# Kernel optimization log

Hardware: AMD Instinct MI355X
Metric: run time of the kernel (lower is better)

Reference implementation:

```python
import jax, jax.numpy as jnp
import numpy as np

EPS = 1e-6  # model.epsilon


def setup_inputs() -> dict:
    key = jax.random.key(0)
    k1, k2 = jax.random.split(key)
    # X: one-hot-like translated sequence tensor [genomes, tiles, 6 frames, tile_len, alphabet]
    X = jax.random.uniform(k1, (8, 12, 6, 2000, 21), dtype=jnp.float32)
    Q = jnp.full((21,), 1.0 / 21.0, dtype=jnp.float32)  # background aa distribution
    # P_logit initialized like log(Q) + noise (matches _getRandomProfiles)
    P_logit = jnp.log(Q)[None, :, None] + 4.0 * jax.random.normal(k2, (8, 21, 48), dtype=jnp.float32)
    return {"X": X, "P_logit": P_logit, "Q": Q}


def reference(X, P_logit, Q):
    # P = softmax over alphabet axis; R = log odds vs background, clamped at epsilon
    P = jax.nn.softmax(P_logit, axis=1)                      # [k, A, U]
    R = jnp.log(jnp.maximum(P / Q[None, :, None], EPS))      # [k, A, U]
    D0, D1, D2, L, A = X.shape
    k, _, U = R.shape
    # conv2d with spatial (L, A), in_ch 1, out_ch U; width window covers full alphabet
    Xr = X.reshape(D0 * D1 * D2, L, A, 1)
    W = R.reshape(k, A, 1, U)
    Z = jax.lax.conv_general_dilated(
        Xr, W, window_strides=(1, 1), padding='VALID',
        dimension_numbers=('NHWC', 'HWIO', 'NHWC'))          # [B, L-k+1, 1, U]
    Z = Z.reshape(D0, D1, D2, L - k + 1, U)                  # [D0, D1, D2, P, U]
    S = jnp.max(Z, axis=(2, 3))                              # max over frames & positions -> [D0, D1, U]
    return (S, R, Z)
```

## Files before the change

### kernel.cpp

```cpp
#include <hip/hip_runtime.h>
#include <math.h>

typedef __attribute__((ext_vector_type(8))) short short8;
typedef __attribute__((ext_vector_type(4))) float f32x4;

#define D0n 8
#define D1n 12
#define D2n 6
#define Ln 2000
#define An 21
#define KPn 8
#define Un 48
#define PPn 1993
#define Bn 576
#define S_SIZE 4608
#define R_SIZE 8064

#define BPn 256
#define TILES 2
#define NBX 4
#define XROWS 264
#define XBUF_BYTES (XROWS * 64)
#define RB_BYTES (384 * 64)
#define BOFF (2 * XBUF_BYTES)
#define RED_OFF (BOFF + RB_BYTES)

__device__ __forceinline__ int swz(int b) { return b ^ ((b >> 2) & 0x70); }

__device__ __forceinline__ unsigned int fkey(float f) {
    unsigned int u = __float_as_uint(f);
    return (u & 0x80000000u) ? ~u : (u | 0x80000000u);
}
__device__ __forceinline__ float funkey(unsigned int k) {
    return __uint_as_float((k & 0x80000000u) ? (k ^ 0x80000000u) : ~k);
}
__device__ __forceinline__ unsigned short f2bf(float v) {
    unsigned int b = __float_as_uint(v);
    return (unsigned short)((b + 0x7FFFu + ((b >> 16) & 1u)) >> 16);
}

#define GLOAD_LDS16(g, l)                                                     \
    __builtin_amdgcn_global_load_lds(                                          \
        (const __attribute__((address_space(1))) void*)(g),                    \
        (__attribute__((address_space(3))) void*)(l), 16, 0, 0)

#define TILE_BARRIER()                                                        \
    do {                                                                      \
        asm volatile("s_waitcnt lgkmcnt(0)" ::: "memory");                    \
        __builtin_amdgcn_s_barrier();                                         \
        asm volatile("" ::: "memory");                                        \
    } while (0)

__global__ void k_profile(const float* __restrict__ P_logit,
                          const float* __restrict__ Q,
                          float* __restrict__ Rout,
                          unsigned short* __restrict__ Rb,
                          unsigned int* __restrict__ Skey) {
    int t = blockIdx.x * blockDim.x + threadIdx.x;
    if (t < S_SIZE) Skey[t] = 0u;
    if (t >= KPn * Un) return;
    int kp = t / Un, u = t % Un;
    const float* pl = P_logit + kp * (An * Un) + u;
    float v[An];
    float m = -INFINITY;
#pragma unroll
    for (int a = 0; a < An; ++a) { v[a] = pl[a * Un]; m = fmaxf(m, v[a]); }
    float s = 0.f;
#pragma unroll
    for (int a = 0; a < An; ++a) { v[a] = expf(v[a] - m); s += v[a]; }
    float inv = 1.f / s;
    int rowp = kp * Un + u;
#pragma unroll
    for (int a = 0; a < An; ++a) {
        float r = logf(fmaxf(v[a] * inv / Q[a], 1e-6f));
        Rout[(kp * An + a) * Un + u] = r;
        Rb[swz(rowp * 64 + a * 2) >> 1] = f2bf(r);
    }
#pragma unroll
    for (int a = An; a < 32; ++a) Rb[swz(rowp * 64 + a * 2) >> 1] = 0;
}

__device__ __forceinline__ void xwrite4(char* xbase, int idx, f32x4 g) {
    int fi = idx * 4;
    int row = fi / An;
    int a = fi - row * An;
#pragma unroll
    for (int e = 0; e < 4; ++e) {
        *(unsigned short*)(xbase + swz(row * 64 + a * 2)) = f2bf(g[e]);
        ++a;
        if (a == An) { a = 0; ++row; }
    }
}

__device__ __forceinline__ void xload(const float* __restrict__ X, int b,
                                      int tp0, int t, f32x4 g[3], int& n4) {
    int rows = min(XROWS, Ln - tp0);
    n4 = rows * An / 4;
    const f32x4* src = (const f32x4*)(X + ((size_t)b * Ln + tp0) * An);
#pragma unroll
    for (int i = 0; i < 3; ++i) {
        int idx = t + i * 512;
        g[i] = (idx < n4) ? src[idx] : (f32x4){0.f, 0.f, 0.f, 0.f};
    }
}

__device__ __forceinline__ void xstore(char* xbase, int t, const f32x4 g[3],
                                       int n4) {
#pragma unroll
    for (int i = 0; i < 3; ++i) {
        int idx = t + i * 512;
        if (idx < n4) xwrite4(xbase, idx, g[i]);
    }
}

__device__ __forceinline__ void qloop8(const char* smem, const char* xb,
                                       int lr, int ls, int pw,
                                       f32x4 acc[3][2]) {
#pragma unroll
    for (int q = 0; q < KPn; ++q) {
        const int rr = q * Un + lr;
        short8 rf0 = *(const short8*)(smem + BOFF + swz(rr * 64 + ls * 16));
        short8 rf1 = *(const short8*)(smem + BOFF + swz((rr + 16) * 64 + ls * 16));
        short8 rf2 = *(const short8*)(smem + BOFF + swz((rr + 32) * 64 + ls * 16));
        const int xr = pw + q + lr;
        short8 xf0 = *(const short8*)(xb + swz(xr * 64 + ls * 16));
        short8 xf1 = *(const short8*)(xb + swz((xr + 16) * 64 + ls * 16));
        acc[0][0] = __builtin_amdgcn_mfma_f32_16x16x32_bf16(rf0, xf0, acc[0][0], 0, 0, 0);
        acc[0][1] = __builtin_amdgcn_mfma_f32_16x16x32_bf16(rf0, xf1, acc[0][1], 0, 0, 0);
        acc[1][0] = __builtin_amdgcn_mfma_f32_16x16x32_bf16(rf1, xf0, acc[1][0], 0, 0, 0);
        acc[1][1] = __builtin_amdgcn_mfma_f32_16x16x32_bf16(rf1, xf1, acc[1][1], 0, 0, 0);
        acc[2][0] = __builtin_amdgcn_mfma_f32_16x16x32_bf16(rf2, xf0, acc[2][0], 0, 0, 0);
        acc[2][1] = __builtin_amdgcn_mfma_f32_16x16x32_bf16(rf2, xf1, acc[2][1], 0, 0, 0);
    }
}

__device__ __forceinline__ void store_tile(float* __restrict__ Z, int b,
                                           int tp0, int pw, int lr, int ls,
                                           const f32x4 acc[3][2],
                                           float smax[3][4]) {
#pragma unroll
    for (int np = 0; np < 2; ++np) {
        int p = tp0 + pw + np * 16 + lr;
        if (p < PPn) {
            float* zp = Z + ((size_t)b * PPn + p) * Un + ls * 4;
#pragma unroll
            for (int nu = 0; nu < 3; ++nu) {
                *(f32x4*)(zp + nu * 16) = acc[nu][np];
#pragma unroll
                for (int r = 0; r < 4; ++r)
                    smax[nu][r] = fmaxf(smax[nu][r], acc[nu][np][r]);
            }
        }
    }
}

__global__ __launch_bounds__(512, 4) void k_conv(
        const float* __restrict__ X,
        const unsigned short* __restrict__ Rb,
        float* __restrict__ Z,
        unsigned int* __restrict__ Skey) {
    __shared__ char smem[RED_OFF + 8 * Un * 4];
    const int b = blockIdx.y;
    const int base_p = blockIdx.x * (TILES * BPn);
    const int t = threadIdx.x;
    const int w = t >> 6;
    const int l = t & 63;
    const int lr = l & 15;
    const int ls = l >> 4;
    const int pw = w * 32;

    {
        const uint4* src = (const uint4*)Rb;
        uint4* dst = (uint4*)(smem + BOFF);
#pragma unroll
        for (int i = 0; i < RB_BYTES / 16 / 512; ++i) {
            int idx = t + i * 512;
            GLOAD_LDS16(src + idx, dst + idx);
        }
    }
    {
        uint4 z4 = {0u, 0u, 0u, 0u};
        uint4* xs = (uint4*)smem;
        for (int i = t; i < 2 * XBUF_BYTES / 16; i += 512) xs[i] = z4;
    }
    f32x4 g[3];
    int n4;
    xload(X, b, base_p, t, g, n4);
    __syncthreads();
    xstore((char*)smem, t, g, n4);
    TILE_BARRIER();

    float smax[3][4];
#pragma unroll
    for (int nu = 0; nu < 3; ++nu)
#pragma unroll
        for (int r = 0; r < 4; ++r) smax[nu][r] = -INFINITY;

    f32x4 acc[3][2];

    xload(X, b, base_p + BPn, t, g, n4);
#pragma unroll
    for (int nu = 0; nu < 3; ++nu)
#pragma unroll
        for (int np = 0; np < 2; ++np) acc[nu][np] = (f32x4){0.f, 0.f, 0.f, 0.f};
    qloop8((const char*)smem, (const char*)smem, lr, ls, pw, acc);
    xstore((char*)smem + XBUF_BYTES, t, g, n4);
    store_tile(Z, b, base_p, pw, lr, ls, acc, smax);
    TILE_BARRIER();

#pragma unroll
    for (int nu = 0; nu < 3; ++nu)
#pragma unroll
        for (int np = 0; np < 2; ++np) acc[nu][np] = (f32x4){0.f, 0.f, 0.f, 0.f};
    qloop8((const char*)smem, (const char*)smem + XBUF_BYTES, lr, ls, pw, acc);
    store_tile(Z, b, base_p + BPn, pw, lr, ls, acc, smax);

    float* red = (float*)(smem + RED_OFF);
#pragma unroll
    for (int nu = 0; nu < 3; ++nu)
#pragma unroll
        for (int r = 0; r < 4; ++r) {
            float v = smax[nu][r];
            v = fmaxf(v, __shfl_xor(v, 1));
            v = fmaxf(v, __shfl_xor(v, 2));
            v = fmaxf(v, __shfl_xor(v, 4));
            v = fmaxf(v, __shfl_xor(v, 8));
            if (lr == 0) red[w * Un + nu * 16 + ls * 4 + r] = v;
        }
    __syncthreads();
    if (t < Un) {
        float m = -INFINITY;
#pragma unroll
        for (int wv = 0; wv < 8; ++wv) m = fmaxf(m, red[wv * Un + t]);
        atomicMax(&Skey[(b / D2n) * Un + t], fkey(m));
    }
}

__global__ void k_decode(unsigned int* __restrict__ Skey) {
    int t = blockIdx.x * blockDim.x + threadIdx.x;
    if (t < S_SIZE) {
        float f = funkey(Skey[t]);
        ((float*)Skey)[t] = f;
    }
}

extern "C" void kernel_launch(void* const* d_in, const int* in_sizes, int n_in,
                              void* d_out, int out_size, void* d_ws, size_t ws_size,
                              hipStream_t stream) {
    const float* X = (const float*)d_in[0];
    const float* P_logit = (const float*)d_in[1];
    const float* Q = (const float*)d_in[2];

    float* S = (float*)d_out;
    float* Rout = S + S_SIZE;
    float* Z = Rout + R_SIZE;
    unsigned short* Rb = (unsigned short*)d_ws;

    k_profile<<<(S_SIZE + 63) / 64, 64, 0, stream>>>(P_logit, Q, Rout, Rb,
                                                     (unsigned int*)d_out);

    dim3 grid(NBX, Bn);
    k_conv<<<grid, 512, 0, stream>>>(X, Rb, Z, (unsigned int*)d_out);

    k_decode<<<(S_SIZE + 255) / 256, 256, 0, stream>>>((unsigned int*)d_out);
}
```

Before: 82.53 us.

## Use persistent blocks processing nine consecutive tiles with double-buffered X loads

Replaces the 4x576 grid of two-tile blocks with 512 persistent blocks, each walking 9 consecutive 256-position tiles across batch boundaries. The next tile's X is prefetched while the current one is computed, and the per-group max is flushed with an atomic only when the genome-tile group changes. This amortizes the per-block R staging into LDS and the launch/prologue cost, and balances the 4608 tiles over 512 blocks. In exchange, the flush adds extra barriers, and a block whose tiles span two groups pays for an additional reduction.

```diff
diff --git a/kernel.cpp b/kernel.cpp
--- a/kernel.cpp
+++ b/kernel.cpp
@@ -17,8 +17,8 @@
 #define R_SIZE 8064
 
 #define BPn 256
-#define TILES 2
-#define NBX 4
+#define NTIL 9
+#define NBLK 512
 #define XROWS 264
 #define XBUF_BYTES (XROWS * 64)
 #define RB_BYTES (384 * 64)
@@ -154,67 +154,10 @@
     }
 }
 
-__global__ __launch_bounds__(512, 4) void k_conv(
-        const float* __restrict__ X,
-        const unsigned short* __restrict__ Rb,
-        float* __restrict__ Z,
-        unsigned int* __restrict__ Skey) {
-    __shared__ char smem[RED_OFF + 8 * Un * 4];
-    const int b = blockIdx.y;
-    const int base_p = blockIdx.x * (TILES * BPn);
-    const int t = threadIdx.x;
-    const int w = t >> 6;
-    const int l = t & 63;
-    const int lr = l & 15;
-    const int ls = l >> 4;
-    const int pw = w * 32;
-
-    {
-        const uint4* src = (const uint4*)Rb;
-        uint4* dst = (uint4*)(smem + BOFF);
-#pragma unroll
-        for (int i = 0; i < RB_BYTES / 16 / 512; ++i) {
-            int idx = t + i * 512;
-            GLOAD_LDS16(src + idx, dst + idx);
-        }
-    }
-    {
-        uint4 z4 = {0u, 0u, 0u, 0u};
-        uint4* xs = (uint4*)smem;
-        for (int i = t; i < 2 * XBUF_BYTES / 16; i += 512) xs[i] = z4;
-    }
-    f32x4 g[3];
-    int n4;
-    xload(X, b, base_p, t, g, n4);
-    __syncthreads();
-    xstore((char*)smem, t, g, n4);
-    TILE_BARRIER();
-
-    float smax[3][4];
-#pragma unroll
-    for (int nu = 0; nu < 3; ++nu)
-#pragma unroll
-        for (int r = 0; r < 4; ++r) smax[nu][r] = -INFINITY;
-
-    f32x4 acc[3][2];
-
-    xload(X, b, base_p + BPn, t, g, n4);
-#pragma unroll
-    for (int nu = 0; nu < 3; ++nu)
-#pragma unroll
-        for (int np = 0; np < 2; ++np) acc[nu][np] = (f32x4){0.f, 0.f, 0.f, 0.f};
-    qloop8((const char*)smem, (const char*)smem, lr, ls, pw, acc);
-    xstore((char*)smem + XBUF_BYTES, t, g, n4);
-    store_tile(Z, b, base_p, pw, lr, ls, acc, smax);
-    TILE_BARRIER();
-
-#pragma unroll
-    for (int nu = 0; nu < 3; ++nu)
-#pragma unroll
-        for (int np = 0; np < 2; ++np) acc[nu][np] = (f32x4){0.f, 0.f, 0.f, 0.f};
-    qloop8((const char*)smem, (const char*)smem + XBUF_BYTES, lr, ls, pw, acc);
-    store_tile(Z, b, base_p + BPn, pw, lr, ls, acc, smax);
-
+__device__ __forceinline__ void flush_smax(char* smem, float smax[3][4],
+                                           int w, int lr, int ls, int t,
+                                           int grp,
+                                           unsigned int* __restrict__ Skey) {
     float* red = (float*)(smem + RED_OFF);
 #pragma unroll
     for (int nu = 0; nu < 3; ++nu)
@@ -226,14 +169,94 @@
             v = fmaxf(v, __shfl_xor(v, 4));
             v = fmaxf(v, __shfl_xor(v, 8));
             if (lr == 0) red[w * Un + nu * 16 + ls * 4 + r] = v;
+            smax[nu][r] = -INFINITY;
         }
     __syncthreads();
     if (t < Un) {
         float m = -INFINITY;
 #pragma unroll
         for (int wv = 0; wv < 8; ++wv) m = fmaxf(m, red[wv * Un + t]);
-        atomicMax(&Skey[(b / D2n) * Un + t], fkey(m));
-    }
+        atomicMax(&Skey[grp * Un + t], fkey(m));
+    }
+    __syncthreads();
+}
+
+__global__ __launch_bounds__(512, 4) void k_conv(
+        const float* __restrict__ X,
+        const unsigned short* __restrict__ Rb,
+        float* __restrict__ Z,
+        unsigned int* __restrict__ Skey) {
+    __shared__ char smem[RED_OFF + 8 * Un * 4];
+    const int gblk = blockIdx.x;
+    const int tau0 = gblk * NTIL;
+    const int t = threadIdx.x;
+    const int w = t >> 6;
+    const int l = t & 63;
+    const int lr = l & 15;
+    const int ls = l >> 4;
+    const int pw = w * 32;
+
+    {
+        const uint4* src = (const uint4*)Rb;
+        uint4* dst = (uint4*)(smem + BOFF);
+#pragma unroll
+        for (int i = 0; i < RB_BYTES / 16 / 512; ++i) {
+            int idx = t + i * 512;
+            GLOAD_LDS16(src + idx, dst + idx);
+        }
+    }
+    {
+        uint4 z4 = {0u, 0u, 0u, 0u};
+        uint4* xs = (uint4*)smem;
+        for (int i = t; i < 2 * XBUF_BYTES / 16; i += 512) xs[i] = z4;
+    }
+    f32x4 g[3];
+    int n4;
+    xload(X, tau0 >> 3, (tau0 & 7) * BPn, t, g, n4);
+    __syncthreads();
+    xstore((char*)smem, t, g, n4);
+    TILE_BARRIER();
+
+    float smax[3][4];
+#pragma unroll
+    for (int nu = 0; nu < 3; ++nu)
+#pragma unroll
+        for (int r = 0; r < 4; ++r) smax[nu][r] = -INFINITY;
+
+    int cur_grp = tau0 / 48;
+    f32x4 acc[3][2];
+
+    for (int i = 0; i < NTIL; ++i) {
+        const int tau = tau0 + i;
+        const int b = tau >> 3;
+        const int p0 = (tau & 7) * BPn;
+        const int grp = tau / 48;
+        if (grp != cur_grp) {
+            flush_smax((char*)smem, smax, w, lr, ls, t, cur_grp, Skey);
+            cur_grp = grp;
+        }
+
+        if (i + 1 < NTIL) {
+            const int taun = tau + 1;
+            xload(X, taun >> 3, (taun & 7) * BPn, t, g, n4);
+        }
+
+#pragma unroll
+        for (int nu = 0; nu < 3; ++nu)
+#pragma unroll
+            for (int np = 0; np < 2; ++np)
+                acc[nu][np] = (f32x4){0.f, 0.f, 0.f, 0.f};
+        qloop8((const char*)smem, (const char*)smem + (i & 1) * XBUF_BYTES,
+               lr, ls, pw, acc);
+
+        if (i + 1 < NTIL)
+            xstore((char*)smem + ((i + 1) & 1) * XBUF_BYTES, t, g, n4);
+
+        store_tile(Z, b, p0, pw, lr, ls, acc, smax);
+        TILE_BARRIER();
+    }
+
+    flush_smax((char*)smem, smax, w, lr, ls, t, cur_grp, Skey);
 }
 
 __global__ void k_decode(unsigned int* __restrict__ Skey) {
@@ -259,8 +282,7 @@
     k_profile<<<(S_SIZE + 63) / 64, 64, 0, stream>>>(P_logit, Q, Rout, Rb,
                                                      (unsigned int*)d_out);
 
-    dim3 grid(NBX, Bn);
-    k_conv<<<grid, 512, 0, stream>>>(X, Rb, Z, (unsigned int*)d_out);
+    k_conv<<<NBLK, 512, 0, stream>>>(X, Rb, Z, (unsigned int*)d_out);
 
     k_decode<<<(S_SIZE + 255) / 256, 256, 0, stream>>>((unsigned int*)d_out);
 }
```

Result: slower. 85.07 us (+3.1%).

## Pre-convert X to padded bf16 buffer and stage tiles via direct LDS loads

Applied to the files above, without the earlier changes.

Adds a separate kernel that converts X from fp32 into a swizzled, 64-byte-padded bf16 workspace buffer. The conv kernel then fills its LDS tiles with async global-to-LDS loads instead of register loads plus per-element bf16 conversion and scattered LDS writes. Z is written with nontemporal stores. The extra pass reads X and writes about 74MB of bf16 data, which the conv kernel then reads back, so total memory traffic increases in exchange for a simpler staging path. The old kernel is kept as a fallback for when the workspace is too small.

```diff
diff --git a/kernel.cpp b/kernel.cpp
--- a/kernel.cpp
+++ b/kernel.cpp
@@ -17,13 +17,16 @@
 #define R_SIZE 8064
 
 #define BPn 256
-#define TILES 2
 #define NBX 4
 #define XROWS 264
 #define XBUF_BYTES (XROWS * 64)
 #define RB_BYTES (384 * 64)
 #define BOFF (2 * XBUF_BYTES)
 #define RED_OFF (BOFF + RB_BYTES)
+
+#define XP_OFF 32768
+#define XP_BYTES ((size_t)Bn * Ln * 64)
+#define WS_NEED (XP_OFF + XP_BYTES)
 
 __device__ __forceinline__ int swz(int b) { return b ^ ((b >> 2) & 0x70); }
 
@@ -80,37 +83,26 @@
     for (int a = An; a < 32; ++a) Rb[swz(rowp * 64 + a * 2) >> 1] = 0;
 }
 
-__device__ __forceinline__ void xwrite4(char* xbase, int idx, f32x4 g) {
-    int fi = idx * 4;
-    int row = fi / An;
-    int a = fi - row * An;
-#pragma unroll
-    for (int e = 0; e < 4; ++e) {
-        *(unsigned short*)(xbase + swz(row * 64 + a * 2)) = f2bf(g[e]);
-        ++a;
-        if (a == An) { a = 0; ++row; }
-    }
-}
-
-__device__ __forceinline__ void xload(const float* __restrict__ X, int b,
-                                      int tp0, int t, f32x4 g[3], int& n4) {
-    int rows = min(XROWS, Ln - tp0);
-    n4 = rows * An / 4;
-    const f32x4* src = (const f32x4*)(X + ((size_t)b * Ln + tp0) * An);
-#pragma unroll
-    for (int i = 0; i < 3; ++i) {
-        int idx = t + i * 512;
-        g[i] = (idx < n4) ? src[idx] : (f32x4){0.f, 0.f, 0.f, 0.f};
-    }
-}
-
-__device__ __forceinline__ void xstore(char* xbase, int t, const f32x4 g[3],
-                                       int n4) {
-#pragma unroll
-    for (int i = 0; i < 3; ++i) {
-        int idx = t + i * 512;
-        if (idx < n4) xwrite4(xbase, idx, g[i]);
-    }
+__global__ __launch_bounds__(256) void k_xconv(const float* __restrict__ X,
+                                               unsigned short* __restrict__ Xp) {
+    int s = blockIdx.x * 256 + threadIdx.x;
+    int R = s >> 2, part = s & 3;
+    unsigned int pk[4];
+    if (part == 3) {
+        pk[0] = pk[1] = pk[2] = pk[3] = 0u;
+    } else {
+        const float* src = X + (size_t)R * An + part * 8;
+        int nv = An - part * 8; if (nv > 8) nv = 8;
+        float f[8];
+#pragma unroll
+        for (int e = 0; e < 8; ++e) f[e] = (e < nv) ? src[e] : 0.f;
+#pragma unroll
+        for (int i2 = 0; i2 < 4; ++i2)
+            pk[i2] = (unsigned int)f2bf(f[2 * i2]) |
+                     ((unsigned int)f2bf(f[2 * i2 + 1]) << 16);
+    }
+    uint4 v = {pk[0], pk[1], pk[2], pk[3]};
+    *(uint4*)((char*)Xp + swz(R * 64 + part * 16)) = v;
 }
 
 __device__ __forceinline__ void qloop8(const char* smem, const char* xb,
@@ -134,6 +126,26 @@
     }
 }
 
+__device__ __forceinline__ void store_tile_nt(float* __restrict__ Z, int b,
+                                              int tp0, int pw, int lr, int ls,
+                                              const f32x4 acc[3][2],
+                                              float smax[3][4]) {
+#pragma unroll
+    for (int np = 0; np < 2; ++np) {
+        int p = tp0 + pw + np * 16 + lr;
+        if (p < PPn) {
+            float* zp = Z + ((size_t)b * PPn + p) * Un + ls * 4;
+#pragma unroll
+            for (int nu = 0; nu < 3; ++nu) {
+                __builtin_nontemporal_store(acc[nu][np], (f32x4*)(zp + nu * 16));
+#pragma unroll
+                for (int r = 0; r < 4; ++r)
+                    smax[nu][r] = fmaxf(smax[nu][r], acc[nu][np][r]);
+            }
+        }
+    }
+}
+
 __device__ __forceinline__ void store_tile(float* __restrict__ Z, int b,
                                            int tp0, int pw, int lr, int ls,
                                            const f32x4 acc[3][2],
@@ -154,14 +166,26 @@
     }
 }
 
-__global__ __launch_bounds__(512, 4) void k_conv(
-        const float* __restrict__ X,
+__device__ __forceinline__ void xstage(const unsigned short* __restrict__ Xp,
+                                       int b, int p0, int t, char* dst) {
+    int rows = min(XROWS, Ln - p0);
+    int slots = rows * 4;
+    const char* src = (const char*)Xp + ((size_t)b * Ln + p0) * 64;
+#pragma unroll
+    for (int i = 0; i < 3; ++i) {
+        int idx = t + i * 512;
+        if (idx < slots) GLOAD_LDS16(src + (size_t)idx * 16, dst + idx * 16);
+    }
+}
+
+__global__ __launch_bounds__(512) void k_conv(
         const unsigned short* __restrict__ Rb,
+        const unsigned short* __restrict__ Xp,
         float* __restrict__ Z,
         unsigned int* __restrict__ Skey) {
     __shared__ char smem[RED_OFF + 8 * Un * 4];
     const int b = blockIdx.y;
-    const int base_p = blockIdx.x * (TILES * BPn);
+    const int base_p = blockIdx.x * (2 * BPn);
     const int t = threadIdx.x;
     const int w = t >> 6;
     const int l = t & 63;
@@ -170,25 +194,16 @@
     const int pw = w * 32;
 
     {
-        const uint4* src = (const uint4*)Rb;
-        uint4* dst = (uint4*)(smem + BOFF);
+        const char* src = (const char*)Rb;
+        char* dst = smem + BOFF;
 #pragma unroll
         for (int i = 0; i < RB_BYTES / 16 / 512; ++i) {
             int idx = t + i * 512;
-            GLOAD_LDS16(src + idx, dst + idx);
-        }
-    }
-    {
-        uint4 z4 = {0u, 0u, 0u, 0u};
-        uint4* xs = (uint4*)smem;
-        for (int i = t; i < 2 * XBUF_BYTES / 16; i += 512) xs[i] = z4;
-    }
-    f32x4 g[3];
-    int n4;
-    xload(X, b, base_p, t, g, n4);
+            GLOAD_LDS16(src + idx * 16, dst + idx * 16);
+        }
+    }
+    xstage(Xp, b, base_p, t, (char*)smem);
     __syncthreads();
-    xstore((char*)smem, t, g, n4);
-    TILE_BARRIER();
 
     float smax[3][4];
 #pragma unroll
@@ -198,22 +213,22 @@
 
     f32x4 acc[3][2];
 
-    xload(X, b, base_p + BPn, t, g, n4);
+    xstage(Xp, b, base_p + BPn, t, (char*)smem + XBUF_BYTES);
 #pragma unroll
     for (int nu = 0; nu < 3; ++nu)
 #pragma unroll
         for (int np = 0; np < 2; ++np) acc[nu][np] = (f32x4){0.f, 0.f, 0.f, 0.f};
     qloop8((const char*)smem, (const char*)smem, lr, ls, pw, acc);
-    xstore((char*)smem + XBUF_BYTES, t, g, n4);
-    store_tile(Z, b, base_p, pw, lr, ls, acc, smax);
-    TILE_BARRIER();
+    asm volatile("s_waitcnt vmcnt(0)" ::: "memory");
+    store_tile_nt(Z, b, base_p, pw, lr, ls, acc, smax);
+    __builtin_amdgcn_s_barrier();
 
 #pragma unroll
     for (int nu = 0; nu < 3; ++nu)
 #pragma unroll
         for (int np = 0; np < 2; ++np) acc[nu][np] = (f32x4){0.f, 0.f, 0.f, 0.f};
     qloop8((const char*)smem, (const char*)smem + XBUF_BYTES, lr, ls, pw, acc);
-    store_tile(Z, b, base_p + BPn, pw, lr, ls, acc, smax);
+    store_tile_nt(Z, b, base_p + BPn, pw, lr, ls, acc, smax);
 
     float* red = (float*)(smem + RED_OFF);
 #pragma unroll
@@ -236,6 +251,121 @@
     }
 }
 
+__device__ __forceinline__ void xwrite4(char* xbase, int idx, f32x4 g) {
+    int fi = idx * 4;
+    int row = fi / An;
+    int a = fi - row * An;
+#pragma unroll
+    for (int e = 0; e < 4; ++e) {
+        *(unsigned short*)(xbase + swz(row * 64 + a * 2)) = f2bf(g[e]);
+        ++a;
+        if (a == An) { a = 0; ++row; }
+    }
+}
+
+__device__ __forceinline__ void xload(const float* __restrict__ X, int b,
+                                      int tp0, int t, f32x4 g[3], int& n4) {
+    int rows = min(XROWS, Ln - tp0);
+    n4 = rows * An / 4;
+    const f32x4* src = (const f32x4*)(X + ((size_t)b * Ln + tp0) * An);
+#pragma unroll
+    for (int i = 0; i < 3; ++i) {
+        int idx = t + i * 512;
+        g[i] = (idx < n4) ? src[idx] : (f32x4){0.f, 0.f, 0.f, 0.f};
+    }
+}
+
+__device__ __forceinline__ void xstore(char* xbase, int t, const f32x4 g[3],
+                                       int n4) {
+#pragma unroll
+    for (int i = 0; i < 3; ++i) {
+        int idx = t + i * 512;
+        if (idx < n4) xwrite4(xbase, idx, g[i]);
+    }
+}
+
+__global__ __launch_bounds__(512, 4) void k_conv_fb(
+        const float* __restrict__ X,
+        const unsigned short* __restrict__ Rb,
+        float* __restrict__ Z,
+        unsigned int* __restrict__ Skey) {
+    __shared__ char smem[RED_OFF + 8 * Un * 4];
+    const int b = blockIdx.y;
+    const int base_p = blockIdx.x * (2 * BPn);
+    const int t = threadIdx.x;
+    const int w = t >> 6;
+    const int l = t & 63;
+    const int lr = l & 15;
+    const int ls = l >> 4;
+    const int pw = w * 32;
+
+    {
+        const char* src = (const char*)Rb;
+        char* dst = smem + BOFF;
+#pragma unroll
+        for (int i = 0; i < RB_BYTES / 16 / 512; ++i) {
+            int idx = t + i * 512;
+            GLOAD_LDS16(src + idx * 16, dst + idx * 16);
+        }
+    }
+    {
+        uint4 z4 = {0u, 0u, 0u, 0u};
+        uint4* xs = (uint4*)smem;
+        for (int i = t; i < 2 * XBUF_BYTES / 16; i += 512) xs[i] = z4;
+    }
+    f32x4 g[3];
+    int n4;
+    xload(X, b, base_p, t, g, n4);
+    __syncthreads();
+    xstore((char*)smem, t, g, n4);
+    TILE_BARRIER();
+
+    float smax[3][4];
+#pragma unroll
+    for (int nu = 0; nu < 3; ++nu)
+#pragma unroll
+        for (int r = 0; r < 4; ++r) smax[nu][r] = -INFINITY;
+
+    f32x4 acc[3][2];
+
+    xload(X, b, base_p + BPn, t, g, n4);
+#pragma unroll
+    for (int nu = 0; nu < 3; ++nu)
+#pragma unroll
+        for (int np = 0; np < 2; ++np) acc[nu][np] = (f32x4){0.f, 0.f, 0.f, 0.f};
+    qloop8((const char*)smem, (const char*)smem, lr, ls, pw, acc);
+    xstore((char*)smem + XBUF_BYTES, t, g, n4);
+    store_tile(Z, b, base_p, pw, lr, ls, acc, smax);
+    TILE_BARRIER();
+
+#pragma unroll
+    for (int nu = 0; nu < 3; ++nu)
+#pragma unroll
+        for (int np = 0; np < 2; ++np) acc[nu][np] = (f32x4){0.f, 0.f, 0.f, 0.f};
+    qloop8((const char*)smem, (const char*)smem + XBUF_BYTES, lr, ls, pw, acc);
+    store_tile(Z, b, base_p + BPn, pw, lr, ls, acc, smax);
+
+    float* red = (float*)(smem + RED_OFF);
+#pragma unroll
+    for (int nu = 0; nu < 3; ++nu)
+#pragma unroll
+        for (int r = 0; r < 4; ++r) {
+            float v = smax[nu][r];
+            v = fmaxf(v, __shfl_xor(v, 1));
+            v = fmaxf(v, __shfl_xor(v, 2));
+            v = fmaxf(v, __shfl_xor(v, 4));
+            v = fmaxf(v, __shfl_xor(v, 8));
+            if (lr == 0) red[w * Un + nu * 16 + ls * 4 + r] = v;
+        }
+    __syncthreads();
+    if (t < Un) {
+        float m = -INFINITY;
+#pragma unroll
+        for (int wv = 0; wv < 8; ++wv) m = fmaxf(m, red[wv * Un + t]);
+        atomicMax(&Skey[(b / D2n) * Un + t], fkey(m));
+    }
+}
+
 __global__ void k_decode(unsigned int* __restrict__ Skey) {
     int t = blockIdx.x * blockDim.x + threadIdx.x;
     if (t < S_SIZE) {
@@ -260,7 +390,13 @@
                                                      (unsigned int*)d_out);
 
     dim3 grid(NBX, Bn);
-    k_conv<<<grid, 512, 0, stream>>>(X, Rb, Z, (unsigned int*)d_out);
+    if (ws_size >= WS_NEED) {
+        unsigned short* Xp = (unsigned short*)((char*)d_ws + XP_OFF);
+        k_xconv<<<(Bn * Ln * 4) / 256, 256, 0, stream>>>(X, Xp);
+        k_conv<<<grid, 512, 0, stream>>>(Rb, Xp, Z, (unsigned int*)d_out);
+    } else {
+        k_conv_fb<<<grid, 512, 0, stream>>>(X, Rb, Z, (unsigned int*)d_out);
+    }
 
     k_decode<<<(S_SIZE + 255) / 256, 256, 0, stream>>>((unsigned int*)d_out);
 }
```

Result: slower. 105.1 us (+27.4%).
